# Kernel tuning notes

Hardware: AMD Instinct MI355X
Metric: run time of the kernel (lower is better)

The kernel has to match this reference:

```python
import jax, jax.numpy as jnp
import numpy as np

EPS = 1e-5

def _layernorm(x, g, b):
    mu = jnp.mean(x, axis=-1, keepdims=True)
    var = jnp.mean(jnp.square(x - mu), axis=-1, keepdims=True)
    return (x - mu) * jax.lax.rsqrt(var + EPS) * g + b

def setup_inputs() -> dict:
    key = jax.random.key(0)
    ks = jax.random.split(key, 6)
    B, S, D = 4, 2048, 1024
    F = 4 * D
    return {
        "hidden_states": jax.random.normal(ks[0], (B, S, D), jnp.float32),
        "w_qkv": jax.random.normal(ks[1], (D, 3 * D), jnp.float32) * (D ** -0.5),
        "fc1_w": jax.random.normal(ks[2], (D, F), jnp.float32) * (D ** -0.5),
        "fc1_b": jax.random.normal(ks[3], (F,), jnp.float32) * 0.02,
        "fc2_w": jax.random.normal(ks[4], (F, D), jnp.float32) * (F ** -0.5),
        "fc2_b": jax.random.normal(ks[5], (D,), jnp.float32) * 0.02,
        "ln1_g": jnp.ones((D,), jnp.float32),
        "ln1_b": jnp.zeros((D,), jnp.float32),
        "ln2_g": jnp.ones((D,), jnp.float32),
        "ln2_b": jnp.zeros((D,), jnp.float32),
    }

def reference(hidden_states, w_qkv, fc1_w, fc1_b, fc2_w, fc2_b, ln1_g, ln1_b, ln2_g, ln2_b):
    D = hidden_states.shape[-1]
    residual = hidden_states
    h = _layernorm(hidden_states, ln1_g, ln1_b)
    qkv = jnp.einsum('bsd,de->bse', h, w_qkv)  # [B,S,3D]
    q, k, v = jnp.split(qkv, 3, axis=-1)
    # single-head attention, NO 1/sqrt(d) scaling, no mask (faithful to source)
    scores = jnp.einsum('bsd,btd->bst', q, k)  # [B,S,S]
    w = jax.nn.softmax(scores, axis=-1)
    attn = jnp.einsum('bst,btd->bsd', w, v)
    h = attn + residual
    residual = h
    h = _layernorm(h, ln2_g, ln2_b)
    h = jnp.einsum('bsd,df->bsf', h, fc1_w) + fc1_b
    h = jax.nn.gelu(h, approximate=False)  # torch nn.GELU default is exact erf
    h = jnp.einsum('bsf,fd->bsd', h, fc2_w) + fc2_b
    return h + residual
```

## Files before the change

kernel.cpp:

```cpp
#include <hip/hip_runtime.h>
#include <math.h>

typedef unsigned short u16;
typedef unsigned int u32;
typedef _Float16 f16x8 __attribute__((ext_vector_type(8)));
typedef float f32x4 __attribute__((ext_vector_type(4)));
typedef u16 u16x4 __attribute__((ext_vector_type(4)));

__device__ __forceinline__ u16 f2h(float x) {
  _Float16 h = (_Float16)x;
  return __builtin_bit_cast(u16, h);
}
__device__ __forceinline__ float h2f(u16 u) {
  return (float)__builtin_bit_cast(_Float16, u);
}

__device__ __forceinline__ float gelu_erf(float x) {
  const float u = x * 0.70710678118654752f;
  const float s = fabsf(u);
  const float t = __frcp_rn(1.0f + 0.3275911f * s);
  float p = 1.061405429f;
  p = p * t - 1.453152027f;
  p = p * t + 1.421413741f;
  p = p * t - 0.284496736f;
  p = p * t + 0.254829592f;
  const float e = __expf(-s * s);
  float erf = 1.0f - p * t * e;
  erf = u < 0.0f ? -erf : erf;
  return 0.5f * x * (1.0f + erf);
}

__device__ __forceinline__ void gload16(const void* g, void* l) {
  __builtin_amdgcn_global_load_lds(
      (const __attribute__((address_space(1))) void*)g,
      (__attribute__((address_space(3))) void*)l, 16, 0, 0);
}

template <int EPI, bool SWZ>
__global__ __launch_bounds__(256, 4) void gemm_nt(
    const u16* __restrict__ A, const u16* __restrict__ B, int M, int N, int K,
    int lda, int ldb, long zsA, long zsB, long zsC, float* __restrict__ outF,
    u16* __restrict__ outU, u16* __restrict__ outU2,
    const float* __restrict__ aux0, const u16* __restrict__ aux1u) {
  __shared__ char smem[2 * 128 * 64 * 2];
  char* sA = smem;
  char* sB = smem + 16384;

  const int tid = threadIdx.x;
  const int lane = tid & 63;
  const int wave = tid >> 6;
  const int z = blockIdx.z;

  int bx = blockIdx.x, by = blockIdx.y;
  if constexpr (SWZ) {
    const int gx = gridDim.x;
    const int nwg = gx * gridDim.y;
    const int id = by * gx + bx;
    const int q = nwg >> 3;
    const int id2 = (id & 7) * q + (id >> 3);
    bx = id2 % gx;
    by = id2 / gx;
  }
  const long row0 = (long)by * 128;
  const long col0 = (long)bx * 128;

  const u16* __restrict__ Ab = A + (long)z * zsA;
  const u16* __restrict__ Bb = B + (long)z * zsB;

  const int srow = lane >> 3;
  const int sslot = (lane & 7) ^ srow;

  const int wm = (wave >> 1) << 6;
  const int wn = (wave & 1) << 6;
  const int fr = lane & 15;
  const int kgrp = lane >> 4;

  f32x4 acc[4][4] = {};
  const int nk = K >> 6;

  auto stage = [&](int kt) {
#pragma unroll
    for (int c = 0; c < 4; ++c) {
      const int chunk = wave * 4 + c;
      const int r = chunk * 8 + srow;
      gload16(Ab + (row0 + r) * (long)lda + kt * 64 + sslot * 8,
              sA + chunk * 1024);
      gload16(Bb + (col0 + r) * (long)ldb + kt * 64 + sslot * 8,
              sB + chunk * 1024);
    }
  };

  stage(0);
  for (int kt = 0; kt < nk; ++kt) {
    __syncthreads();
#pragma unroll
    for (int kk = 0; kk < 2; ++kk) {
      f16x8 af[4], bg[4];
#pragma unroll
      for (int i = 0; i < 4; ++i) {
        const int r = wm + i * 16 + fr;
        const int slot = ((kk << 2) | kgrp) ^ (r & 7);
        af[i] = *(const f16x8*)(sA + r * 128 + slot * 16);
      }
#pragma unroll
      for (int j = 0; j < 4; ++j) {
        const int r = wn + j * 16 + fr;
        const int slot = ((kk << 2) | kgrp) ^ (r & 7);
        bg[j] = *(const f16x8*)(sB + r * 128 + slot * 16);
      }
#pragma unroll
      for (int i = 0; i < 4; ++i)
#pragma unroll
        for (int j = 0; j < 4; ++j)
          acc[i][j] = __builtin_amdgcn_mfma_f32_16x16x32_f16(af[i], bg[j],
                                                             acc[i][j], 0, 0, 0);
    }
    __syncthreads();
    if (kt + 1 < nk) stage(kt + 1);
  }

#pragma unroll
  for (int i = 0; i < 4; ++i) {
    const long m0 = row0 + wm + i * 16 + (kgrp << 2);
#pragma unroll
    for (int j = 0; j < 4; ++j) {
      const long n = col0 + wn + j * 16 + fr;
      if constexpr (EPI == 0) {
        if (n < 2048) {
#pragma unroll
          for (int r = 0; r < 4; ++r)
            outU[(m0 + r) * 2048 + n] = f2h(acc[i][j][r]);
        } else {
          u16x4 V;
#pragma unroll
          for (int r = 0; r < 4; ++r) V[r] = f2h(acc[i][j][r]);
          *(u16x4*)(outU2 + ((m0 >> 11) << 21) + (n - 2048) * 2048 +
                    (m0 & 2047)) = V;
        }
      } else if constexpr (EPI == 1) {
#pragma unroll
        for (int r = 0; r < 4; ++r)
          outF[(long)z * zsC + (m0 + r) * (long)N + n] = acc[i][j][r];
      } else if constexpr (EPI == 2) {
#pragma unroll
        for (int r = 0; r < 4; ++r) {
          const long idx = (long)z * zsC + (m0 + r) * (long)N + n;
          outU[idx] = f2h(acc[i][j][r] + aux0[idx]);
        }
      } else if constexpr (EPI == 3) {
        const float b = aux0[n];
#pragma unroll
        for (int r = 0; r < 4; ++r)
          outU[(m0 + r) * (long)N + n] = f2h(gelu_erf(acc[i][j][r] + b));
      } else {
        const float b = aux0[n];
#pragma unroll
        for (int r = 0; r < 4; ++r) {
          const long idx = (m0 + r) * (long)N + n;
          outF[idx] = acc[i][j][r] + b + h2f(aux1u[idx]);
        }
      }
    }
  }
}

template <bool F32IN>
__global__ __launch_bounds__(256) void ln_k(const void* __restrict__ xin,
                                            const float* __restrict__ gw,
                                            const float* __restrict__ bw,
                                            u16* __restrict__ out) {
  const int lane = threadIdx.x & 63;
  const int wv = threadIdx.x >> 6;
  const long row = (long)blockIdx.x * 4 + wv;
  float4 v[4];
  float s = 0.f, ss = 0.f;
#pragma unroll
  for (int j = 0; j < 4; ++j) {
    const int n = (lane + 64 * j) * 4;
    if constexpr (F32IN) {
      v[j] = *(const float4*)((const float*)xin + row * 1024 + n);
    } else {
      const u16x4 hv = *(const u16x4*)((const u16*)xin + row * 1024 + n);
      v[j] = make_float4(h2f(hv[0]), h2f(hv[1]), h2f(hv[2]), h2f(hv[3]));
    }
    s += v[j].x + v[j].y + v[j].z + v[j].w;
    ss += v[j].x * v[j].x + v[j].y * v[j].y + v[j].z * v[j].z + v[j].w * v[j].w;
  }
#pragma unroll
  for (int o = 32; o; o >>= 1) {
    s += __shfl_xor(s, o);
    ss += __shfl_xor(ss, o);
  }
  const float mu = s * (1.f / 1024.f);
  const float var = ss * (1.f / 1024.f) - mu * mu;
  const float rs = rsqrtf(var + 1e-5f);
  u16* orow = out + row * 1024;
#pragma unroll
  for (int j = 0; j < 4; ++j) {
    const int n = (lane + 64 * j) * 4;
    const float4 gg = *(const float4*)(gw + n);
    const float4 bb = *(const float4*)(bw + n);
    u16x4 H;
    H[0] = f2h((v[j].x - mu) * rs * gg.x + bb.x);
    H[1] = f2h((v[j].y - mu) * rs * gg.y + bb.y);
    H[2] = f2h((v[j].z - mu) * rs * gg.z + bb.z);
    H[3] = f2h((v[j].w - mu) * rs * gg.w + bb.w);
    *(u16x4*)(orow + n) = H;
  }
}

__global__ __launch_bounds__(256) void transpose_k(const float* __restrict__ in,
                                                   u16* __restrict__ out,
                                                   int R, int C) {
  __shared__ float tile[32][33];
  const int c0 = blockIdx.x * 32, r0 = blockIdx.y * 32;
#pragma unroll
  for (int i = 0; i < 4; ++i) {
    const int lin = threadIdx.x + 256 * i;
    const int rr = lin >> 5, cc = lin & 31;
    tile[rr][cc] = in[(long)(r0 + rr) * C + c0 + cc];
  }
  __syncthreads();
#pragma unroll
  for (int i = 0; i < 4; ++i) {
    const int lin = threadIdx.x + 256 * i;
    const int oc = lin >> 5, orr = lin & 31;
    out[(long)(c0 + oc) * R + (r0 + orr)] = f2h(tile[orr][oc]);
  }
}

__global__ __launch_bounds__(256) void softmax_k(float* __restrict__ S) {
  const long row = blockIdx.x;
  float* sr = S + row * 2048;
  u16* pr = (u16*)sr;
  const int tid = threadIdx.x;
  const int lane = tid & 63, wv = tid >> 6;
  __shared__ float red[8];
  const float4 v0 = *(const float4*)(sr + tid * 4);
  const float4 v1 = *(const float4*)(sr + 1024 + tid * 4);
  float mx = fmaxf(fmaxf(fmaxf(v0.x, v0.y), fmaxf(v0.z, v0.w)),
                   fmaxf(fmaxf(v1.x, v1.y), fmaxf(v1.z, v1.w)));
#pragma unroll
  for (int o = 32; o; o >>= 1) mx = fmaxf(mx, __shfl_xor(mx, o));
  if (lane == 0) red[wv] = mx;
  __syncthreads();
  mx = fmaxf(fmaxf(red[0], red[1]), fmaxf(red[2], red[3]));
  float e[8];
  e[0] = __expf(v0.x - mx); e[1] = __expf(v0.y - mx);
  e[2] = __expf(v0.z - mx); e[3] = __expf(v0.w - mx);
  e[4] = __expf(v1.x - mx); e[5] = __expf(v1.y - mx);
  e[6] = __expf(v1.z - mx); e[7] = __expf(v1.w - mx);
  float sm = e[0] + e[1] + e[2] + e[3] + e[4] + e[5] + e[6] + e[7];
#pragma unroll
  for (int o = 32; o; o >>= 1) sm += __shfl_xor(sm, o);
  if (lane == 0) red[4 + wv] = sm;
  __syncthreads();
  sm = red[4] + red[5] + red[6] + red[7];
  const float inv = 1.f / sm;
  u16x4 a, b;
  a[0] = f2h(e[0] * inv); a[1] = f2h(e[1] * inv);
  a[2] = f2h(e[2] * inv); a[3] = f2h(e[3] * inv);
  b[0] = f2h(e[4] * inv); b[1] = f2h(e[5] * inv);
  b[2] = f2h(e[6] * inv); b[3] = f2h(e[7] * inv);
  *(u16x4*)(pr + tid * 4) = a;
  *(u16x4*)(pr + 1024 + tid * 4) = b;
}

extern "C" void kernel_launch(void* const* d_in, const int* in_sizes, int n_in,
                              void* d_out, int out_size, void* d_ws,
                              size_t ws_size, hipStream_t stream) {
  const float* x     = (const float*)d_in[0];
  const float* w_qkv = (const float*)d_in[1];
  const float* fc1_w = (const float*)d_in[2];
  const float* fc1_b = (const float*)d_in[3];
  const float* fc2_w = (const float*)d_in[4];
  const float* fc2_b = (const float*)d_in[5];
  const float* ln1_g = (const float*)d_in[6];
  const float* ln1_b = (const float*)d_in[7];
  const float* ln2_g = (const float*)d_in[8];
  const float* ln2_b = (const float*)d_in[9];
  float* out = (float*)d_out;

  char* ws = (char*)d_ws;
  const long MB = 1024L * 1024L;
  u16*   h    = (u16*)(ws + 0);
  u16*   wqkT = (u16*)(ws + 16 * MB);
  float* sc   = (float*)(ws + 0);
  u16*   qk   = (u16*)(ws + 64 * MB);
  u16*   h2   = (u16*)(ws + 96 * MB);
  u16*   vT   = (u16*)(ws + 112 * MB);
  u16*   w1T  = (u16*)(ws + 144 * MB);
  u16*   w2T  = (u16*)(ws + 152 * MB);
  u16*   r2   = (u16*)(ws + 160 * MB);
  u16*   g    = (u16*)(ws + 0);

  dim3 blk(256);

  ln_k<true><<<2048, blk, 0, stream>>>(x, ln1_g, ln1_b, h);
  transpose_k<<<dim3(3072 / 32, 1024 / 32, 1), blk, 0, stream>>>(w_qkv, wqkT,
                                                                 1024, 3072);
  gemm_nt<0, true><<<dim3(24, 64, 1), blk, 0, stream>>>(
      h, wqkT, 8192, 3072, 1024, 1024, 1024, 0, 0, 0, nullptr, qk, vT,
      nullptr, nullptr);
  gemm_nt<1, true><<<dim3(16, 16, 4), blk, 0, stream>>>(
      qk, qk + 1024, 2048, 2048, 1024, 2048, 2048, 2048L * 2048, 2048L * 2048,
      2048L * 2048, sc, nullptr, nullptr, nullptr, nullptr);
  softmax_k<<<8192, blk, 0, stream>>>(sc);
  gemm_nt<2, true><<<dim3(8, 16, 4), blk, 0, stream>>>(
      (const u16*)sc, vT, 2048, 1024, 2048, 4096, 2048, 2048L * 4096,
      1024L * 2048, 2048L * 1024, nullptr, r2, nullptr, x, nullptr);
  ln_k<false><<<2048, blk, 0, stream>>>(r2, ln2_g, ln2_b, h2);
  transpose_k<<<dim3(4096 / 32, 1024 / 32, 1), blk, 0, stream>>>(fc1_w, w1T,
                                                                 1024, 4096);
  transpose_k<<<dim3(1024 / 32, 4096 / 32, 1), blk, 0, stream>>>(fc2_w, w2T,
                                                                 4096, 1024);
  gemm_nt<3, true><<<dim3(32, 64, 1), blk, 0, stream>>>(
      h2, w1T, 8192, 4096, 1024, 1024, 1024, 0, 0, 0, nullptr, g, nullptr,
      fc1_b, nullptr);
  gemm_nt<4, true><<<dim3(8, 64, 1), blk, 0, stream>>>(
      g, w2T, 8192, 1024, 4096, 4096, 4096, 0, 0, 0, out, nullptr, nullptr,
      fc2_b, r2);
}
```

Before: 369.7 us.

## Add 8-wave large-tile GEMM kernel with phased prefetch for MLP layers

Adds a new 512-thread GEMM kernel with 256-row tiles, 64*JF-column tiles and dynamic LDS double buffering. It splits each K-step into phases that interleave direct-to-LDS global loads with MFMA work, using sched barriers, explicit waitcnt and setprio. The fc1 (GELU epilogue) and fc2 (bias plus residual epilogue) GEMMs now use it instead of the 128x128 kernel. The aim is more data reuse per block and better overlap of loads with math, at the cost of more LDS per block, which lowers occupancy.

```diff
diff --git a/kernel.cpp b/kernel.cpp
--- a/kernel.cpp
+++ b/kernel.cpp
@@ -36,6 +36,8 @@
       (__attribute__((address_space(3))) void*)l, 16, 0, 0);
 }
 
+#define SGB() __builtin_amdgcn_sched_barrier(0)
+
 template <int EPI, bool SWZ>
 __global__ __launch_bounds__(256, 4) void gemm_nt(
     const u16* __restrict__ A, const u16* __restrict__ B, int M, int N, int K,
@@ -148,6 +150,172 @@
           outU[idx] = f2h(acc[i][j][r] + aux0[idx]);
         }
       } else if constexpr (EPI == 3) {
+        const float b = aux0[n];
+#pragma unroll
+        for (int r = 0; r < 4; ++r)
+          outU[(m0 + r) * (long)N + n] = f2h(gelu_erf(acc[i][j][r] + b));
+      } else {
+        const float b = aux0[n];
+#pragma unroll
+        for (int r = 0; r < 4; ++r) {
+          const long idx = (m0 + r) * (long)N + n;
+          outF[idx] = acc[i][j][r] + b + h2f(aux1u[idx]);
+        }
+      }
+    }
+  }
+}
+
+template <int JF, int NPH, int EPI, bool SWZ>
+__global__ __launch_bounds__(512, 2) void gemm8f(
+    const u16* __restrict__ A, const u16* __restrict__ B, int M, int N, int K,
+    int lda, int ldb, float* __restrict__ outF, u16* __restrict__ outU,
+    const float* __restrict__ aux0, const u16* __restrict__ aux1u) {
+  constexpr int BUF = 32768 + JF * 8192;
+  constexpr int IPP = 8 / NPH;
+  extern __shared__ __align__(16) char smem[];
+
+  const int tid = threadIdx.x;
+  const int lane = tid & 63;
+  const int wave = tid >> 6;
+
+  int bx = blockIdx.x, by = blockIdx.y;
+  if constexpr (SWZ) {
+    const int gx = gridDim.x;
+    const int nwg = gx * gridDim.y;
+    const int id = by * gx + bx;
+    const int q = nwg >> 3;
+    const int id2 = (id & 7) * q + (id >> 3);
+    bx = id2 % gx;
+    by = id2 / gx;
+  }
+  const long row0 = (long)by * 256;
+  const long col0 = (long)bx * (64 * JF);
+
+  const int srow = lane >> 3;
+  const int gslot = (lane & 7) ^ srow;
+  const int fr = lane & 15;
+  const int kgrp = lane >> 4;
+  const int wm = (wave >> 2) << 7;
+  const int wn = (wave & 3) * (16 * JF);
+
+  const int nk = K >> 6;
+
+  const int slot0 = kgrp ^ (fr & 7);
+  const int offA0 = (wm + fr) * 128 + slot0 * 16;
+  const int offA1 = offA0 ^ 64;
+  const int offB0 = 32768 + (wn + fr) * 128 + slot0 * 16;
+  const int offB1 = offB0 ^ 64;
+
+  const u16* const gA0 = A + (row0 + wave * 16 + srow) * (long)lda + gslot * 8;
+  const u16* const gA1 = gA0 + 128 * (long)lda;
+  const u16* const gB0 = B + (col0 + wave * 16 + srow) * (long)ldb + gslot * 8;
+  const u16* const gB1 = gB0 + 128 * (long)ldb;
+  char* const dA = smem + wave * 2048 + lane * 16;
+  char* const dB = dA + 32768;
+
+  f32x4 acc[8][JF] = {};
+  f16x8 bfrag[2][JF];
+
+  auto stageA = [&](int buf, int kt, int h) {
+    const long ko = (long)kt * 64;
+    const u16* g = (h ? gA1 : gA0) + ko;
+    char* d = dA + buf * BUF + (h ? 16384 : 0);
+    gload16(g, d);
+    gload16(g + 8 * (long)lda, d + 1024);
+  };
+  auto stageB = [&](int buf, int kt, int h) {
+    const long ko = (long)kt * 64;
+    const u16* g = (h ? gB1 : gB0) + ko;
+    char* d = dB + buf * BUF + (h ? 16384 : 0);
+    gload16(g, d);
+    gload16(g + 8 * (long)ldb, d + 1024);
+  };
+
+  stageA(0, 0, 0);
+  stageA(0, 0, 1);
+  stageB(0, 0, 0);
+  if constexpr (JF == 4) stageB(0, 0, 1);
+  stageB(1, 1, 0);
+  if constexpr (JF == 4) stageB(1, 1, 1);
+  SGB();
+  if constexpr (JF == 4)
+    asm volatile("s_waitcnt vmcnt(4)" ::: "memory");
+  else
+    asm volatile("s_waitcnt vmcnt(2)" ::: "memory");
+  SGB();
+  __builtin_amdgcn_s_barrier();
+
+  for (int s = 0; s < nk; ++s) {
+    const int cur = s & 1;
+    const bool stA = (s + 1 < nk);
+    const bool stB = (s + 2 < nk);
+    const char* sb = smem + cur * BUF;
+    const char* pA0 = sb + offA0;
+    const char* pA1 = sb + offA1;
+    const char* pB0 = sb + offB0;
+    const char* pB1 = sb + offB1;
+#pragma unroll
+    for (int p = 0; p < NPH; ++p) {
+      f16x8 af[IPP][2];
+#pragma unroll
+      for (int ii = 0; ii < IPP; ++ii) {
+        af[ii][0] = *(const f16x8*)(pA0 + (p * IPP + ii) * 2048);
+        af[ii][1] = *(const f16x8*)(pA1 + (p * IPP + ii) * 2048);
+      }
+      if (p == 0) {
+#pragma unroll
+        for (int j = 0; j < JF; ++j) {
+          bfrag[0][j] = *(const f16x8*)(pB0 + j * 2048);
+          bfrag[1][j] = *(const f16x8*)(pB1 + j * 2048);
+        }
+      }
+      SGB();
+      if (p == 0 && stA) stageA(cur ^ 1, s + 1, 0);
+      if (p == 1) {
+        if (stA) stageA(cur ^ 1, s + 1, 1);
+        if (stB) stageB(cur, s + 2, 0);
+      }
+      if constexpr (NPH == 4) {
+        if (p == 2 && stB) stageB(cur, s + 2, 1);
+      }
+      SGB();
+      __builtin_amdgcn_s_barrier();
+      asm volatile("s_waitcnt lgkmcnt(0)" ::: "memory");
+      SGB();
+      __builtin_amdgcn_s_setprio(1);
+#pragma unroll
+      for (int kk = 0; kk < 2; ++kk)
+#pragma unroll
+        for (int ii = 0; ii < IPP; ++ii)
+#pragma unroll
+          for (int j = 0; j < JF; ++j)
+            acc[p * IPP + ii][j] = __builtin_amdgcn_mfma_f32_16x16x32_f16(
+                af[ii][kk], bfrag[kk][j], acc[p * IPP + ii][j], 0, 0, 0);
+      __builtin_amdgcn_s_setprio(0);
+      SGB();
+      if (p == NPH - 1) {
+        if (stB) {
+          if constexpr (JF == 4)
+            asm volatile("s_waitcnt vmcnt(4)" ::: "memory");
+          else
+            asm volatile("s_waitcnt vmcnt(2)" ::: "memory");
+        } else {
+          asm volatile("s_waitcnt vmcnt(0)" ::: "memory");
+        }
+        SGB();
+      }
+      __builtin_amdgcn_s_barrier();
+    }
+  }
+
+#pragma unroll
+  for (int i = 0; i < 8; ++i) {
+#pragma unroll
+    for (int j = 0; j < JF; ++j) {
+      const long n = col0 + wn + j * 16 + fr;
+      const long m0 = row0 + wm + i * 16 + (kgrp << 2);
+      if constexpr (EPI == 3) {
         const float b = aux0[n];
 #pragma unroll
         for (int r = 0; r < 4; ++r)
@@ -295,6 +463,13 @@
   u16*   g    = (u16*)(ws + 0);
 
   dim3 blk(256);
+  dim3 blk8(512);
+  const int LDS4 = 131072;
+  const int LDS2 = 98304;
+  (void)hipFuncSetAttribute((const void*)gemm8f<4, 4, 3, true>,
+                            hipFuncAttributeMaxDynamicSharedMemorySize, LDS4);
+  (void)hipFuncSetAttribute((const void*)gemm8f<2, 2, 4, true>,
+                            hipFuncAttributeMaxDynamicSharedMemorySize, LDS2);
 
   ln_k<true><<<2048, blk, 0, stream>>>(x, ln1_g, ln1_b, h);
   transpose_k<<<dim3(3072 / 32, 1024 / 32, 1), blk, 0, stream>>>(w_qkv, wqkT,
@@ -314,10 +489,8 @@
                                                                  1024, 4096);
   transpose_k<<<dim3(1024 / 32, 4096 / 32, 1), blk, 0, stream>>>(fc2_w, w2T,
                                                                  4096, 1024);
-  gemm_nt<3, true><<<dim3(32, 64, 1), blk, 0, stream>>>(
-      h2, w1T, 8192, 4096, 1024, 1024, 1024, 0, 0, 0, nullptr, g, nullptr,
-      fc1_b, nullptr);
-  gemm_nt<4, true><<<dim3(8, 64, 1), blk, 0, stream>>>(
-      g, w2T, 8192, 1024, 4096, 4096, 4096, 0, 0, 0, out, nullptr, nullptr,
-      fc2_b, r2);
-}
+  gemm8f<4, 4, 3, true><<<dim3(16, 32, 1), blk8, LDS4, stream>>>(
+      h2, w1T, 8192, 4096, 1024, 1024, 1024, nullptr, g, fc1_b, nullptr);
+  gemm8f<2, 2, 4, true><<<dim3(8, 32, 1), blk8, LDS2, stream>>>(
+      g, w2T, 8192, 1024, 4096, 4096, 4096, out, nullptr, fc2_b, r2);
+}
```

Result: slower. 384.7 us (+4.1%).

## Fold Wq·Wkᵀ into a single weight to cut QKV projection work

Applied to the files above, without the earlier changes.

Rewrites the scores as h·(Wq Wkᵀ)·hᵀ. A small 1024x1024 GEMM precomputes Wq·Wkᵀ, and the QKV GEMM then outputs only t = h·W and V, so N drops from 3072 to 2048. The score GEMM now uses t and h directly. This adds a small weight GEMM plus conversion kernels and changes the rounding path, since products go through fp16 at a different point, which may hurt accuracy given the unscaled softmax.

```diff
diff --git a/kernel.cpp b/kernel.cpp
--- a/kernel.cpp
+++ b/kernel.cpp
@@ -126,15 +126,15 @@
     for (int j = 0; j < 4; ++j) {
       const long n = col0 + wn + j * 16 + fr;
       if constexpr (EPI == 0) {
-        if (n < 2048) {
+        if (n < 1024) {
 #pragma unroll
           for (int r = 0; r < 4; ++r)
-            outU[(m0 + r) * 2048 + n] = f2h(acc[i][j][r]);
+            outU[(m0 + r) * 1024 + n] = f2h(acc[i][j][r]);
         } else {
           u16x4 V;
 #pragma unroll
           for (int r = 0; r < 4; ++r) V[r] = f2h(acc[i][j][r]);
-          *(u16x4*)(outU2 + ((m0 >> 11) << 21) + (n - 2048) * 2048 +
+          *(u16x4*)(outU2 + ((m0 >> 11) << 21) + (n - 1024) * 2048 +
                     (m0 & 2047)) = V;
         }
       } else if constexpr (EPI == 1) {
@@ -152,13 +152,17 @@
 #pragma unroll
         for (int r = 0; r < 4; ++r)
           outU[(m0 + r) * (long)N + n] = f2h(gelu_erf(acc[i][j][r] + b));
-      } else {
+      } else if constexpr (EPI == 4) {
         const float b = aux0[n];
 #pragma unroll
         for (int r = 0; r < 4; ++r) {
           const long idx = (m0 + r) * (long)N + n;
           outF[idx] = acc[i][j][r] + b + h2f(aux1u[idx]);
         }
+      } else {
+#pragma unroll
+        for (int r = 0; r < 4; ++r)
+          outU[(m0 + r) * (long)N + n] = f2h(acc[i][j][r]);
       }
     }
   }
@@ -227,6 +231,17 @@
     const int oc = lin >> 5, orr = lin & 31;
     out[(long)(c0 + oc) * R + (r0 + orr)] = f2h(tile[orr][oc]);
   }
+}
+
+__global__ __launch_bounds__(256) void convert_k(const float* __restrict__ in,
+                                                 u16* __restrict__ out) {
+  const int idx = blockIdx.x * 256 + threadIdx.x;
+  const int row = idx >> 9;
+  const int c = (idx & 511) * 4;
+  const float4 v = *(const float4*)(in + (long)row * 3072 + c);
+  u16x4 H;
+  H[0] = f2h(v.x); H[1] = f2h(v.y); H[2] = f2h(v.z); H[3] = f2h(v.w);
+  *(u16x4*)(out + (long)row * 2048 + c) = H;
 }
 
 __global__ __launch_bounds__(256) void softmax_k(float* __restrict__ S) {
@@ -283,27 +298,33 @@
 
   char* ws = (char*)d_ws;
   const long MB = 1024L * 1024L;
-  u16*   h    = (u16*)(ws + 0);
-  u16*   wqkT = (u16*)(ws + 16 * MB);
-  float* sc   = (float*)(ws + 0);
-  u16*   qk   = (u16*)(ws + 64 * MB);
-  u16*   h2   = (u16*)(ws + 96 * MB);
-  u16*   vT   = (u16*)(ws + 112 * MB);
-  u16*   w1T  = (u16*)(ws + 144 * MB);
-  u16*   w2T  = (u16*)(ws + 152 * MB);
-  u16*   r2   = (u16*)(ws + 160 * MB);
-  u16*   g    = (u16*)(ws + 0);
+  u16*   h      = (u16*)(ws + 0);
+  u16*   wqk_rm = (u16*)(ws + 16 * MB);
+  u16*   W2     = (u16*)(ws + 20 * MB);
+  u16*   wvT    = (u16*)(ws + 22 * MB);
+  u16*   t      = (u16*)(ws + 24 * MB);
+  u16*   vT     = (u16*)(ws + 40 * MB);
+  float* sc     = (float*)(ws + 64 * MB);
+  u16*   r2     = (u16*)(ws + 128 * MB);
+  u16*   h2     = (u16*)(ws + 144 * MB);
+  u16*   w1T    = (u16*)(ws + 160 * MB);
+  u16*   w2T    = (u16*)(ws + 168 * MB);
+  u16*   g      = (u16*)(ws + 0);
 
   dim3 blk(256);
 
   ln_k<true><<<2048, blk, 0, stream>>>(x, ln1_g, ln1_b, h);
-  transpose_k<<<dim3(3072 / 32, 1024 / 32, 1), blk, 0, stream>>>(w_qkv, wqkT,
-                                                                 1024, 3072);
-  gemm_nt<0, true><<<dim3(24, 64, 1), blk, 0, stream>>>(
-      h, wqkT, 8192, 3072, 1024, 1024, 1024, 0, 0, 0, nullptr, qk, vT,
-      nullptr, nullptr);
+  convert_k<<<2048, blk, 0, stream>>>(w_qkv, wqk_rm);
+  transpose_k<<<dim3(1024 / 32, 1024 / 32, 1), blk, 0, stream>>>(
+      w_qkv + 2048, wvT, 1024, 3072);
+  gemm_nt<5, true><<<dim3(8, 8, 1), blk, 0, stream>>>(
+      wqk_rm + 1024, wqk_rm, 1024, 1024, 1024, 2048, 2048, 0, 0, 0, nullptr,
+      W2, nullptr, nullptr, nullptr);
+  gemm_nt<0, true><<<dim3(16, 64, 1), blk, 0, stream>>>(
+      h, W2, 8192, 2048, 1024, 1024, 1024, 0, 0, 0, nullptr, t, vT, nullptr,
+      nullptr);
   gemm_nt<1, true><<<dim3(16, 16, 4), blk, 0, stream>>>(
-      qk, qk + 1024, 2048, 2048, 1024, 2048, 2048, 2048L * 2048, 2048L * 2048,
+      t, h, 2048, 2048, 1024, 1024, 1024, 2048L * 1024, 2048L * 1024,
       2048L * 2048, sc, nullptr, nullptr, nullptr, nullptr);
   softmax_k<<<8192, blk, 0, stream>>>(sc);
   gemm_nt<2, true><<<dim3(8, 16, 4), blk, 0, stream>>>(
```

Result: no change. 370.5 us (+0.2%).
